# Optimization experiments

Measured on AMD Instinct MI355X. Metric: run time of the kernel, lower is better.

The kernel has to match this reference:

```python
import jax, jax.numpy as jnp
import numpy as np

TAU = 0.1          # temperature from init_kwargs
EPS = 1e-8         # torch.nn.CosineSimilarity default eps


def setup_inputs() -> dict:
    key = jax.random.key(0)
    k1, k2, k3 = jax.random.split(key, 3)
    B, D = 2048, 128
    return {
        "z_i": jax.random.normal(k1, (B, D), dtype=jnp.float32),
        "z_j": jax.random.normal(k2, (B, D), dtype=jnp.float32),
        "y": jax.random.randint(k3, (B,), 0, 10, dtype=jnp.int64),
    }


def reference(z_i, z_j, y):
    # p: (2N, D)
    p = jnp.concatenate([z_i, z_j], axis=0)
    n2 = p.shape[0]
    # Cosine similarity via norms + single GEMM (same math as pairwise
    # CosineSimilarity: dot / max(||a||*||b||, eps)), then temperature scale.
    norms = jnp.linalg.norm(p, axis=1)                      # (2N,)
    sim = (p @ p.T) / jnp.maximum(norms[:, None] * norms[None, :], EPS) / TAU

    # Positive mask: same label, diagonal removed.
    y2 = jnp.concatenate([y, y], axis=0)                    # (2N,)
    off_diag = 1.0 - jnp.eye(n2, dtype=sim.dtype)           # logit mask
    mask = (y2[:, None] == y2[None, :]).astype(sim.dtype) * off_diag

    # Masked log-softmax over each row (self excluded from denominator).
    exp_logits = jnp.exp(sim) * off_diag
    log_prob = sim - jnp.log(exp_logits.sum(axis=1, keepdims=True))

    mean_log_prob_pos = (mask * log_prob).sum(axis=1) / mask.sum(axis=1)
    return -mean_log_prob_pos.mean()
```

## Files before the change

### kernel.cpp

```cpp
#include <hip/hip_runtime.h>

#define N2 4096
#define D 128
#define TAU_INV 10.0f
#define JSL 4
#define TPW (N2 / (JSL * 128))
#define GEMM_BLOCKS (128 * JSL)
#define NCLS 10
#define CGRP 16
#define CROWS (N2 / CGRP)
#define CB (NCLS * CGRP)

typedef __attribute__((ext_vector_type(8))) short bf16x8;
typedef __attribute__((ext_vector_type(16))) float floatx16;

__device__ __forceinline__ short f2bf(float f) {
    unsigned u = __float_as_uint(f);
    u = (u + 0x7fff + ((u >> 16) & 1)) >> 16;
    return (short)u;
}
__device__ __forceinline__ float bf2f(short s) {
    return __uint_as_float(((unsigned)(unsigned short)s) << 16);
}

__global__ __launch_bounds__(64) void prep_kernel(const float* __restrict__ zi,
                                                  const float* __restrict__ zj,
                                                  short* __restrict__ qb,
                                                  float* __restrict__ se_g,
                                                  float* __restrict__ S) {
    int row = blockIdx.x;
    int lane = threadIdx.x;
    const float* src = (row < 2048) ? (zi + row * D) : (zj + (row - 2048) * D);
    float2 v = ((const float2*)src)[lane];
    float ss = v.x * v.x + v.y * v.y;
    #pragma unroll
    for (int m = 1; m < 64; m <<= 1) ss += __shfl_xor(ss, m);
    float inv = 1.0f / sqrtf(ss);
    short2 o;
    o.x = f2bf(v.x * inv);
    o.y = f2bf(v.y * inv);
    ((short2*)(qb + row * D))[lane] = o;
    if (lane == 0) se_g[row] = 0.f;
    if (row == 0)
        for (int k = lane; k < NCLS * D + 2 * NCLS; k += 64) S[k] = 0.f;
}

__global__ __launch_bounds__(256) void main_kernel(const short* __restrict__ qb,
                                                   const long long* __restrict__ y,
                                                   float* __restrict__ se_g,
                                                   float* __restrict__ S) {
    int tid = threadIdx.x;

    if (blockIdx.x >= GEMM_BLOCKS) {
        int cb = blockIdx.x - GEMM_BLOCKS;
        int c  = cb / CGRP;
        int g  = cb % CGRP;
        int d  = tid & 127;
        int rh = tid >> 7;
        int r0 = g * CROWS + rh * (CROWS / 2);

        float sS = 0.f, sT = 0.f, cnt = 0.f;
        #pragma unroll 4
        for (int i = 0; i < CROWS / 2; ++i) {
            int r = r0 + i;
            bool m = ((int)y[r & 2047] == c);
            float q = bf2f(qb[r * D + d]);
            sS += m ? q : 0.f;
            sT += m ? q * q : 0.f;
            cnt += m ? 1.f : 0.f;
        }

        __shared__ float shS[256];
        __shared__ float shT[4];
        __shared__ float shC[2];
        shS[tid] = sS;
        #pragma unroll
        for (int m = 1; m < 64; m <<= 1) sT += __shfl_xor(sT, m);
        if ((tid & 63) == 0) shT[tid >> 6] = sT;
        if (d == 0) shC[rh] = cnt;
        __syncthreads();
        if (tid < 128) atomicAdd(&S[c * D + tid], shS[tid] + shS[tid + 128]);
        if (tid == 0) {
            atomicAdd(&S[NCLS * D + c], shT[0] + shT[1] + shT[2] + shT[3]);
            atomicAdd(&S[NCLS * D + NCLS + c], shC[0] + shC[1]);
        }
        return;
    }

    int wave = tid >> 6;
    int lane = tid & 63;
    int col  = lane & 31;
    int half = lane >> 5;
    int it = blockIdx.x >> 2;
    int js = blockIdx.x & (JSL - 1);
    int i0 = it * 32;
    int jbase = js * (N2 / JSL);

    const short* ap = qb + (i0 + col) * D + half * 8;
    bf16x8 af[8];
    #pragma unroll
    for (int k = 0; k < 8; ++k) af[k] = *(const bf16x8*)(ap + k * 16);

    float se[16];
    #pragma unroll
    for (int r = 0; r < 16; ++r) se[r] = 0.f;

    bf16x8 bf[8];
    {
        const short* bp = qb + (jbase + wave * 32 + col) * D + half * 8;
        #pragma unroll
        for (int k = 0; k < 8; ++k) bf[k] = *(const bf16x8*)(bp + k * 16);
    }

    #pragma unroll
    for (int t = 0; t < TPW; ++t) {
        int j0 = jbase + (wave + 4 * t) * 32;

        bf16x8 bn[8];
        if (t < TPW - 1) {
            const short* bp = qb + (j0 + 128 + col) * D + half * 8;
            #pragma unroll
            for (int k = 0; k < 8; ++k) bn[k] = *(const bf16x8*)(bp + k * 16);
        }

        floatx16 acc;
        #pragma unroll
        for (int r = 0; r < 16; ++r) acc[r] = 0.f;
        #pragma unroll
        for (int k = 0; k < 8; ++k)
            acc = __builtin_amdgcn_mfma_f32_32x32x16_bf16(af[k], bf[k], acc, 0, 0, 0);

        if (j0 == i0) {
            int jcol = j0 + col;
            #pragma unroll
            for (int r = 0; r < 16; ++r) {
                int rowr = i0 + (r & 3) + 8 * (r >> 2) + 4 * half;
                float e = __expf(acc[r] * TAU_INV);
                se[r] += (rowr == jcol) ? 0.f : e;
            }
        } else {
            #pragma unroll
            for (int r = 0; r < 16; ++r)
                se[r] += __expf(acc[r] * TAU_INV);
        }

        if (t < TPW - 1) {
            #pragma unroll
            for (int k = 0; k < 8; ++k) bf[k] = bn[k];
        }
    }

    #pragma unroll
    for (int r = 0; r < 16; ++r) {
        float a = se[r];
        #pragma unroll
        for (int m = 1; m < 32; m <<= 1) a += __shfl_xor(a, m);
        if (col == 0) {
            int rowr = i0 + (r & 3) + 8 * (r >> 2) + 4 * half;
            atomicAdd(&se_g[rowr], a);
        }
    }
}

__global__ __launch_bounds__(256) void finish_kernel(const float* __restrict__ se_g,
                                                     const float* __restrict__ S,
                                                     float* __restrict__ out) {
    int tid = threadIdx.x;
    int wave = tid >> 6;
    int lane = tid & 63;

    float P = 0.f;
    for (int c = wave; c < NCLS; c += 4) {
        float2 sv = ((const float2*)(S + c * D))[lane];
        float s2 = sv.x * sv.x + sv.y * sv.y;
        #pragma unroll
        for (int m = 1; m < 64; m <<= 1) s2 += __shfl_xor(s2, m);
        float n = S[NCLS * D + NCLS + c];
        P += (n >= 2.0f) ? (s2 - S[NCLS * D + c]) * TAU_INV / (n - 1.0f) : 0.f;
    }

    float L = 0.f;
    for (int i = tid; i < N2; i += 256) L += __logf(se_g[i]);
    #pragma unroll
    for (int m = 1; m < 64; m <<= 1) L += __shfl_xor(L, m);

    __shared__ float red[8];
    if (lane == 0) { red[wave] = L; red[4 + wave] = P; }
    __syncthreads();
    if (tid == 0) {
        float Ls = red[0] + red[1] + red[2] + red[3];
        float Ps = red[4] + red[5] + red[6] + red[7];
        out[0] = (Ls - Ps) * (1.0f / (float)N2);
    }
}

extern "C" void kernel_launch(void* const* d_in, const int* in_sizes, int n_in,
                              void* d_out, int out_size, void* d_ws, size_t ws_size,
                              hipStream_t stream) {
    const float*     zi = (const float*)d_in[0];
    const float*     zj = (const float*)d_in[1];
    const long long* y  = (const long long*)d_in[2];
    float* out = (float*)d_out;

    char* ws = (char*)d_ws;
    short* qb   = (short*)ws;
    float* se_g = (float*)(ws + N2 * D * sizeof(short));
    float* S    = se_g + N2;

    prep_kernel<<<N2, 64, 0, stream>>>(zi, zj, qb, se_g, S);
    main_kernel<<<GEMM_BLOCKS + CB, 256, 0, stream>>>(qb, y, se_g, S);
    finish_kernel<<<1, 256, 0, stream>>>(se_g, S, out);
}
```

Before: 98.55 us.

## Switch similarity GEMM to 16x16x32 MFMA tiles with finer column split

Rewrites the fused GEMM+exp-sum path to use 16x16x32 bf16 MFMA tiles: each wave now owns 16 rows and walks 128 columns, and the grid grows to 2048 GEMM blocks. The class-sum blocks are moved to the front of the grid. exp is computed with a native exp2 and a pre-scaled constant, and launch bounds request 6 waves per SIMD. The aim is more parallelism and lower register pressure, so more blocks stay resident. In exchange, the A fragment is reused less, B tiles are loaded without prefetch, and more atomics hit se_g.

```diff
diff --git a/kernel.cpp b/kernel.cpp
--- a/kernel.cpp
+++ b/kernel.cpp
@@ -3,16 +3,16 @@
 #define N2 4096
 #define D 128
 #define TAU_INV 10.0f
-#define JSL 4
-#define TPW (N2 / (JSL * 128))
-#define GEMM_BLOCKS (128 * JSL)
+#define E2SCALE 14.4269504088896340736f
+#define JS 32
+#define GEMM_BLOCKS (64 * JS)
 #define NCLS 10
 #define CGRP 16
 #define CROWS (N2 / CGRP)
 #define CB (NCLS * CGRP)
 
 typedef __attribute__((ext_vector_type(8))) short bf16x8;
-typedef __attribute__((ext_vector_type(16))) float floatx16;
+typedef __attribute__((ext_vector_type(4))) float floatx4;
 
 __device__ __forceinline__ short f2bf(float f) {
     unsigned u = __float_as_uint(f);
@@ -45,14 +45,14 @@
         for (int k = lane; k < NCLS * D + 2 * NCLS; k += 64) S[k] = 0.f;
 }
 
-__global__ __launch_bounds__(256) void main_kernel(const short* __restrict__ qb,
-                                                   const long long* __restrict__ y,
-                                                   float* __restrict__ se_g,
-                                                   float* __restrict__ S) {
+__global__ __launch_bounds__(256, 6) void main_kernel(const short* __restrict__ qb,
+                                                      const long long* __restrict__ y,
+                                                      float* __restrict__ se_g,
+                                                      float* __restrict__ S) {
     int tid = threadIdx.x;
 
-    if (blockIdx.x >= GEMM_BLOCKS) {
-        int cb = blockIdx.x - GEMM_BLOCKS;
+    if (blockIdx.x < CB) {
+        int cb = blockIdx.x;
         int c  = cb / CGRP;
         int g  = cb % CGRP;
         int d  = tid & 127;
@@ -87,78 +87,67 @@
         return;
     }
 
+    int gb = blockIdx.x - CB;
     int wave = tid >> 6;
     int lane = tid & 63;
-    int col  = lane & 31;
-    int half = lane >> 5;
-    int it = blockIdx.x >> 2;
-    int js = blockIdx.x & (JSL - 1);
-    int i0 = it * 32;
-    int jbase = js * (N2 / JSL);
-
-    const short* ap = qb + (i0 + col) * D + half * 8;
-    bf16x8 af[8];
-    #pragma unroll
-    for (int k = 0; k < 8; ++k) af[k] = *(const bf16x8*)(ap + k * 16);
-
-    float se[16];
-    #pragma unroll
-    for (int r = 0; r < 16; ++r) se[r] = 0.f;
-
-    bf16x8 bf[8];
-    {
-        const short* bp = qb + (jbase + wave * 32 + col) * D + half * 8;
-        #pragma unroll
-        for (int k = 0; k < 8; ++k) bf[k] = *(const bf16x8*)(bp + k * 16);
-    }
-
-    #pragma unroll
-    for (int t = 0; t < TPW; ++t) {
-        int j0 = jbase + (wave + 4 * t) * 32;
-
-        bf16x8 bn[8];
-        if (t < TPW - 1) {
-            const short* bp = qb + (j0 + 128 + col) * D + half * 8;
+    int rlo  = lane & 15;
+    int khi  = lane >> 4;
+    int it = gb >> 5;
+    int js = gb & (JS - 1);
+    int rbase = it * 64 + wave * 16;
+    int jbase = js * 128;
+
+    const short* aptr = qb + (rbase + rlo) * D + khi * 8;
+    bf16x8 af[4];
+    #pragma unroll
+    for (int kk = 0; kk < 4; ++kk) af[kk] = *(const bf16x8*)(aptr + kk * 32);
+
+    float se0 = 0.f, se1 = 0.f, se2 = 0.f, se3 = 0.f;
+
+    #pragma unroll
+    for (int t = 0; t < 8; ++t) {
+        int j0 = jbase + t * 16;
+        const short* bptr = qb + (j0 + rlo) * D + khi * 8;
+        bf16x8 b0 = *(const bf16x8*)(bptr);
+        bf16x8 b1 = *(const bf16x8*)(bptr + 32);
+        bf16x8 b2 = *(const bf16x8*)(bptr + 64);
+        bf16x8 b3 = *(const bf16x8*)(bptr + 96);
+
+        floatx4 acc = {0.f, 0.f, 0.f, 0.f};
+        acc = __builtin_amdgcn_mfma_f32_16x16x32_bf16(af[0], b0, acc, 0, 0, 0);
+        acc = __builtin_amdgcn_mfma_f32_16x16x32_bf16(af[1], b1, acc, 0, 0, 0);
+        acc = __builtin_amdgcn_mfma_f32_16x16x32_bf16(af[2], b2, acc, 0, 0, 0);
+        acc = __builtin_amdgcn_mfma_f32_16x16x32_bf16(af[3], b3, acc, 0, 0, 0);
+
+        if (j0 == rbase) {
             #pragma unroll
-            for (int k = 0; k < 8; ++k) bn[k] = *(const bf16x8*)(bp + k * 16);
-        }
-
-        floatx16 acc;
-        #pragma unroll
-        for (int r = 0; r < 16; ++r) acc[r] = 0.f;
-        #pragma unroll
-        for (int k = 0; k < 8; ++k)
-            acc = __builtin_amdgcn_mfma_f32_32x32x16_bf16(af[k], bf[k], acc, 0, 0, 0);
-
-        if (j0 == i0) {
-            int jcol = j0 + col;
-            #pragma unroll
-            for (int r = 0; r < 16; ++r) {
-                int rowr = i0 + (r & 3) + 8 * (r >> 2) + 4 * half;
-                float e = __expf(acc[r] * TAU_INV);
-                se[r] += (rowr == jcol) ? 0.f : e;
+            for (int r = 0; r < 4; ++r) {
+                float e = __builtin_amdgcn_exp2f(acc[r] * E2SCALE);
+                e = (khi * 4 + r == rlo) ? 0.f : e;
+                if (r == 0) se0 += e; else if (r == 1) se1 += e;
+                else if (r == 2) se2 += e; else se3 += e;
             }
         } else {
-            #pragma unroll
-            for (int r = 0; r < 16; ++r)
-                se[r] += __expf(acc[r] * TAU_INV);
+            se0 += __builtin_amdgcn_exp2f(acc[0] * E2SCALE);
+            se1 += __builtin_amdgcn_exp2f(acc[1] * E2SCALE);
+            se2 += __builtin_amdgcn_exp2f(acc[2] * E2SCALE);
+            se3 += __builtin_amdgcn_exp2f(acc[3] * E2SCALE);
         }
-
-        if (t < TPW - 1) {
-            #pragma unroll
-            for (int k = 0; k < 8; ++k) bf[k] = bn[k];
-        }
-    }
-
-    #pragma unroll
-    for (int r = 0; r < 16; ++r) {
-        float a = se[r];
-        #pragma unroll
-        for (int m = 1; m < 32; m <<= 1) a += __shfl_xor(a, m);
-        if (col == 0) {
-            int rowr = i0 + (r & 3) + 8 * (r >> 2) + 4 * half;
-            atomicAdd(&se_g[rowr], a);
-        }
+    }
+
+    #pragma unroll
+    for (int m = 1; m < 16; m <<= 1) {
+        se0 += __shfl_xor(se0, m);
+        se1 += __shfl_xor(se1, m);
+        se2 += __shfl_xor(se2, m);
+        se3 += __shfl_xor(se3, m);
+    }
+    if (rlo == 0) {
+        int rowr = rbase + khi * 4;
+        atomicAdd(&se_g[rowr + 0], se0);
+        atomicAdd(&se_g[rowr + 1], se1);
+        atomicAdd(&se_g[rowr + 2], se2);
+        atomicAdd(&se_g[rowr + 3], se3);
     }
 }
 
@@ -208,6 +197,6 @@
     float* S    = se_g + N2;
 
     prep_kernel<<<N2, 64, 0, stream>>>(zi, zj, qb, se_g, S);
-    main_kernel<<<GEMM_BLOCKS + CB, 256, 0, stream>>>(qb, y, se_g, S);
+    main_kernel<<<CB + GEMM_BLOCKS, 256, 0, stream>>>(qb, y, se_g, S);
     finish_kernel<<<1, 256, 0, stream>>>(se_g, S, out);
 }
```

Result: slower. 112.8 us (+14.4%).
